# Performance work log

Measured on AMD Instinct MI355X. Metric: run time of the kernel, lower is better.

The kernel has to match this reference:

```python
import jax, jax.numpy as jnp
import numpy as np

B, L, D_MODEL = 2, 4096, 256
EXPAND = 2
D_INNER = EXPAND * D_MODEL
D_STATE = 16
D_CONV = 4
DT_RANK = max(1, D_MODEL // 16)


def setup_inputs() -> dict:
    key = jax.random.key(0)
    ks = jax.random.split(key, 8)
    s = 0.02
    return {
        "x": jax.random.normal(ks[0], (B, L, D_MODEL), jnp.float32),
        "in_proj_w": jax.random.normal(ks[1], (D_MODEL, 2 * D_INNER), jnp.float32) * s,
        "conv_w": jax.random.normal(ks[2], (D_INNER, D_CONV), jnp.float32) * 0.1,
        "conv_b": jnp.zeros((D_INNER,), jnp.float32),
        "x_proj_w": jax.random.normal(ks[3], (D_INNER, DT_RANK + 2 * D_STATE), jnp.float32) * s,
        "dt_proj_w": jax.random.normal(ks[4], (DT_RANK, D_INNER), jnp.float32) * (DT_RANK ** -0.5),
        "dt_proj_b": jnp.log(jnp.expm1(jnp.full((D_INNER,), 0.01, jnp.float32))),
        "A_log": jnp.log(jnp.tile(jnp.arange(1, D_STATE + 1, dtype=jnp.float32), (D_INNER, 1))),
        "D": jnp.ones((D_INNER,), jnp.float32),
        "out_proj_w": jax.random.normal(ks[5], (D_INNER, D_MODEL), jnp.float32) * s,
        "ln_gamma": jnp.ones((D_MODEL,), jnp.float32),
        "ln_beta": jnp.zeros((D_MODEL,), jnp.float32),
    }


def _mamba(x, in_proj_w, conv_w, conv_b, x_proj_w, dt_proj_w, dt_proj_b, A_log, D, out_proj_w):
    b = x.shape[0]
    xz = x @ in_proj_w                       # [B,L,2*d_inner]
    u, z = jnp.split(xz, 2, axis=-1)
    # depthwise causal conv over time
    u_pad = jnp.pad(u, ((0, 0), (D_CONV - 1, 0), (0, 0)))
    kern = conv_w.T[:, None, :]              # [D_CONV, 1, D_INNER]
    u_conv = jax.lax.conv_general_dilated(
        u_pad, kern, (1,), 'VALID',
        dimension_numbers=('NHC', 'HIO', 'NHC'),
        feature_group_count=D_INNER) + conv_b
    u_conv = jax.nn.silu(u_conv)             # [B,L,d_inner]
    dbl = u_conv @ x_proj_w
    dt, Bm, Cm = jnp.split(dbl, [DT_RANK, DT_RANK + D_STATE], axis=-1)
    delta = jax.nn.softplus(dt @ dt_proj_w + dt_proj_b)   # [B,L,d_inner]
    A = -jnp.exp(A_log)                                    # [d_inner,d_state]
    dA = jnp.exp(delta[..., None] * A)                     # [B,L,di,ds]
    dBu = delta[..., None] * Bm[:, :, None, :] * u_conv[..., None]

    def step(h, inputs):
        dA_t, dBu_t, C_t = inputs
        h = dA_t * h + dBu_t                 # [B,di,ds]
        y = jnp.einsum('bdn,bn->bd', h, C_t)
        return h, y

    h0 = jnp.zeros((b, D_INNER, D_STATE), u_conv.dtype)
    _, ys = jax.lax.scan(step, h0,
                         (dA.transpose(1, 0, 2, 3),
                          dBu.transpose(1, 0, 2, 3),
                          Cm.transpose(1, 0, 2)))
    y = ys.transpose(1, 0, 2) + u_conv * D
    y = y * jax.nn.silu(z)
    return y @ out_proj_w


def reference(x, in_proj_w, conv_w, conv_b, x_proj_w, dt_proj_w, dt_proj_b,
              A_log, D, out_proj_w, ln_gamma, ln_beta):
    y = x + _mamba(x, in_proj_w, conv_w, conv_b, x_proj_w, dt_proj_w,
                   dt_proj_b, A_log, D, out_proj_w)
    mu = jnp.mean(y, axis=-1, keepdims=True)
    var = jnp.var(y, axis=-1, keepdims=True)
    return (y - mu) / jnp.sqrt(var + 1e-5) * ln_gamma + ln_beta
```

## Files before the change

### kernel.cpp

```cpp
#include <hip/hip_runtime.h>
#include <math.h>

constexpr int BATCH  = 2;
constexpr int LSEQ   = 4096;
constexpr int DMODEL = 256;
constexpr int DINNER = 512;
constexpr int NST    = 16;
constexpr int MROWS  = BATCH * LSEQ;
constexpr int NCH    = 256;
constexpr int TCH    = LSEQ / NCH;
constexpr float LOG2E = 1.44269504088896f;
constexpr float LN2   = 0.69314718056f;

typedef __attribute__((ext_vector_type(8))) short bf16x8;
typedef __attribute__((ext_vector_type(4))) float f32x4;

__device__ __forceinline__ float fast_silu(float v) { return v / (1.f + __expf(-v)); }

__device__ __forceinline__ unsigned short f2bf(float f) {
  unsigned int u = __float_as_uint(f);
  u = (u + 0x7fffu + ((u >> 16) & 1u)) >> 16;
  return (unsigned short)u;
}
__device__ __forceinline__ float bf2f(unsigned short u) {
  return __uint_as_float(((unsigned int)u) << 16);
}

__global__ __launch_bounds__(256) void k_castT(const float* __restrict__ W,
                                               unsigned short* __restrict__ Wt,
                                               int K, int N, int ktiles) {
  __shared__ float tile[32][33];
  const int bt = blockIdx.x;
  const int kt = bt % ktiles, nt = bt / ktiles;
  const int k0 = kt * 32, n0 = nt * 32;
  const int t = threadIdx.x;
  const int c = t & 31, r0 = t >> 5;
  #pragma unroll
  for (int it = 0; it < 4; ++it) {
    int r = r0 + it * 8;
    tile[r][c] = W[(size_t)(k0 + r) * N + n0 + c];
  }
  __syncthreads();
  #pragma unroll
  for (int it = 0; it < 4; ++it) {
    int cc = r0 + it * 8;
    Wt[(size_t)(n0 + cc) * K + k0 + c] = f2bf(tile[c][cc]);
  }
}

__global__ __launch_bounds__(256) void k_cast_xpw(const float* __restrict__ xpw,
                                                  unsigned short* __restrict__ xpT) {
  int idx = blockIdx.x * 256 + threadIdx.x;
  int n = idx >> 9, k = idx & 511;
  xpT[n * 512 + k] = f2bf(xpw[k * 48 + n]);
}

__global__ __launch_bounds__(256) void k_prep_a2(const float* __restrict__ Alog,
                                                 float* __restrict__ a2T) {
  int idx = blockIdx.x * 256 + threadIdx.x;
  int n = idx >> 9, d = idx & 511;
  a2T[idx] = -__expf(Alog[d * NST + n]) * LOG2E;
}

__global__ __launch_bounds__(256) void k_inproj(const float* __restrict__ X,
                                                const unsigned short* __restrict__ Wt,
                                                unsigned short* __restrict__ ub,
                                                unsigned short* __restrict__ zb) {
  __shared__ unsigned short As[128][40];
  __shared__ unsigned short Bs[128][40];
  const int t = threadIdx.x;
  const int m0 = (blockIdx.x & 63) * 128;
  const int n0 = (blockIdx.x >> 6) * 128;
  const int lane = t & 63, wid = t >> 6;
  const int hi = lane >> 4, l15 = lane & 15;
  const int wm = wid >> 1, wn = wid & 1;
  f32x4 zero = {0.f, 0.f, 0.f, 0.f};
  f32x4 acc[4][4];
  #pragma unroll
  for (int i = 0; i < 4; ++i)
    #pragma unroll
    for (int j = 0; j < 4; ++j) acc[i][j] = zero;

  for (int k0 = 0; k0 < DMODEL; k0 += 32) {
    __syncthreads();
    #pragma unroll
    for (int it = 0; it < 4; ++it) {
      int v = it * 256 + t;
      int r = v >> 3, part = v & 7;
      float4 a = *(const float4*)(X + (size_t)(m0 + r) * 256 + k0 + part * 4);
      ushort4 o;
      o.x = f2bf(a.x); o.y = f2bf(a.y); o.z = f2bf(a.z); o.w = f2bf(a.w);
      *(ushort4*)(&As[r][part * 4]) = o;
    }
    #pragma unroll
    for (int it = 0; it < 2; ++it) {
      int v = it * 256 + t;
      int r = v >> 2, part = v & 3;
      *(float4*)(&Bs[r][part * 8]) = *(const float4*)(Wt + (size_t)(n0 + r) * 256 + k0 + part * 8);
    }
    __syncthreads();
    bf16x8 af[4], bfv[4];
    #pragma unroll
    for (int am = 0; am < 4; ++am) af[am] = *(const bf16x8*)(&As[wm * 64 + am * 16 + l15][hi * 8]);
    #pragma unroll
    for (int bn = 0; bn < 4; ++bn) bfv[bn] = *(const bf16x8*)(&Bs[wn * 64 + bn * 16 + l15][hi * 8]);
    #pragma unroll
    for (int am = 0; am < 4; ++am)
      #pragma unroll
      for (int bn = 0; bn < 4; ++bn)
        acc[am][bn] = __builtin_amdgcn_mfma_f32_16x16x32_bf16(af[am], bfv[bn], acc[am][bn], 0, 0, 0);
  }

  unsigned short* dst = (n0 < DINNER) ? ub : zb;
  const int nb = (n0 < DINNER) ? n0 : n0 - DINNER;
  #pragma unroll
  for (int am = 0; am < 4; ++am)
    #pragma unroll
    for (int j = 0; j < 4; ++j) {
      int m = m0 + wm * 64 + am * 16 + hi * 4 + j;
      #pragma unroll
      for (int bn = 0; bn < 4; ++bn) {
        int n = nb + wn * 64 + bn * 16 + l15;
        dst[(size_t)m * DINNER + n] = f2bf(acc[am][bn][j]);
      }
    }
}

__global__ __launch_bounds__(256) void k_conv(const unsigned short* __restrict__ ub,
                                              const float* __restrict__ cw,
                                              const float* __restrict__ cb,
                                              unsigned short* __restrict__ ucb) {
  const int e2 = blockIdx.x * 256 + threadIdx.x;
  const int idx = e2 * 2;
  const int d = idx & (DINNER - 1);
  const int m = idx >> 9;
  const int l = m & (LSEQ - 1);
  float a0 = cb[d], a1 = cb[d + 1];
  #pragma unroll
  for (int j = 0; j < 4; ++j) {
    int lj = l + j - 3;
    unsigned int p = (lj >= 0) ? *(const unsigned int*)(ub + idx + (j - 3) * DINNER) : 0u;
    float u0 = bf2f((unsigned short)(p & 0xffffu));
    float u1 = bf2f((unsigned short)(p >> 16));
    a0 = fmaf(u0, cw[d * 4 + j], a0);
    a1 = fmaf(u1, cw[(d + 1) * 4 + j], a1);
  }
  unsigned int o = (unsigned int)f2bf(fast_silu(a0)) | ((unsigned int)f2bf(fast_silu(a1)) << 16);
  *(unsigned int*)(ucb + idx) = o;
}

__global__ __launch_bounds__(128) void k_xprojm(const unsigned short* __restrict__ ucb,
                                                const unsigned short* __restrict__ xpT,
                                                float* __restrict__ dt_out,
                                                float* __restrict__ Bout,
                                                float* __restrict__ Cout) {
  __shared__ unsigned short As[32][136];
  __shared__ unsigned short Bs[48][136];
  const int t = threadIdx.x;
  const int m0 = blockIdx.x * 32;
  const int lane = t & 63, wid = t >> 6;
  const int hi = lane >> 4, l15 = lane & 15;
  f32x4 zero = {0.f, 0.f, 0.f, 0.f};
  f32x4 acc[3] = {zero, zero, zero};

  for (int k0 = 0; k0 < DINNER; k0 += 128) {
    __syncthreads();
    #pragma unroll
    for (int it = 0; it < 4; ++it) {
      int v = it * 128 + t;
      int r = v >> 4, part = v & 15;
      *(float4*)(&As[r][part * 8]) = *(const float4*)(ucb + (size_t)(m0 + r) * 512 + k0 + part * 8);
    }
    #pragma unroll
    for (int it = 0; it < 6; ++it) {
      int v = it * 128 + t;
      int r = v >> 4, part = v & 15;
      *(float4*)(&Bs[r][part * 8]) = *(const float4*)(xpT + (size_t)r * 512 + k0 + part * 8);
    }
    __syncthreads();
    #pragma unroll
    for (int kk = 0; kk < 4; ++kk) {
      bf16x8 af = *(const bf16x8*)(&As[wid * 16 + l15][kk * 32 + hi * 8]);
      #pragma unroll
      for (int nf = 0; nf < 3; ++nf) {
        bf16x8 bv = *(const bf16x8*)(&Bs[nf * 16 + l15][kk * 32 + hi * 8]);
        acc[nf] = __builtin_amdgcn_mfma_f32_16x16x32_bf16(af, bv, acc[nf], 0, 0, 0);
      }
    }
  }
  #pragma unroll
  for (int j = 0; j < 4; ++j) {
    int m = m0 + wid * 16 + hi * 4 + j;
    dt_out[m * 16 + l15] = acc[0][j];
    Bout[m * 16 + l15]   = acc[1][j];
    Cout[m * 16 + l15]   = acc[2][j];
  }
}

__global__ __launch_bounds__(256) void k_scan1(const unsigned short* __restrict__ ucb,
                                               const float* __restrict__ dtin,
                                               const float* __restrict__ dtw,
                                               const float* __restrict__ dtb,
                                               const float* __restrict__ Bin,
                                               const float* __restrict__ a2T,
                                               unsigned short* __restrict__ delta_b,
                                               unsigned short* __restrict__ Ssum,
                                               float* __restrict__ Dsum) {
  const int t = threadIdx.x;
  const int d0 = (blockIdx.x & 1) * 256;
  const int rest = blockIdx.x >> 1;
  const int c = rest & (NCH - 1);
  const int b = rest >> 8;
  const int d = d0 + t;
  __shared__ float Bsh[TCH][NST];
  __shared__ float dtsh[TCH][NST];
  __shared__ unsigned short UC[TCH][256];
  const int rbase = (b * LSEQ + c * TCH) * DINNER + d0;
  {
    const int base = (b * LSEQ + c * TCH) * NST;
    ((float*)Bsh)[t]  = Bin[base + t];
    ((float*)dtsh)[t] = dtin[base + t];
    #pragma unroll
    for (int it = 0; it < 2; ++it) {
      int v = it * 256 + t;
      int r = v >> 5, col8 = v & 31;
      *(float4*)(&UC[r][col8 * 8]) = *(const float4*)(ucb + rbase + r * DINNER + col8 * 8);
    }
  }
  __syncthreads();
  float dwreg[NST];
  #pragma unroll
  for (int r = 0; r < NST; ++r) dwreg[r] = dtw[r * DINNER + d];
  const float bias = dtb[d];
  float a2[NST];
  #pragma unroll
  for (int n = 0; n < NST; ++n) a2[n] = a2T[n * DINNER + d];
  bool geo = true;
  #pragma unroll
  for (int n = 1; n < NST; ++n)
    geo = geo && (fabsf(a2[n] - (float)(n + 1) * a2[0]) <= 1e-5f * fabsf(a2[n]));
  float S[NST];
  #pragma unroll
  for (int n = 0; n < NST; ++n) S[n] = 0.f;
  float dsum = 0.f;
  const int row0 = rbase + t;
  for (int tt = 0; tt < TCH; ++tt) {
    float acc = bias;
    #pragma unroll
    for (int r = 0; r < NST; ++r) acc = fmaf(dtsh[tt][r], dwreg[r], acc);
    float sp = (acc > 20.f) ? acc : log1pf(__expf(acc));
    unsigned short deb = f2bf(sp);
    delta_b[row0 + tt * DINNER] = deb;
    float de = bf2f(deb);
    float xv = bf2f(UC[tt][t]);
    float du = de * xv;
    dsum += de;
    float dA[NST];
    if (geo) {
      float r1 = exp2f(de * a2[0]);
      float p = r1;
      #pragma unroll
      for (int n = 0; n < NST; ++n) { dA[n] = p; p *= r1; }
    } else {
      #pragma unroll
      for (int n = 0; n < NST; ++n) dA[n] = exp2f(de * a2[n]);
    }
    #pragma unroll
    for (int n = 0; n < NST; ++n) S[n] = fmaf(dA[n], S[n], du * Bsh[tt][n]);
  }
  const int bc = b * NCH + c;
  Dsum[bc * DINNER + d] = dsum;
  #pragma unroll
  for (int n = 0; n < NST; ++n)
    Ssum[(size_t)((n * BATCH + b) * NCH + c) * DINNER + d] = f2bf(S[n]);
}

__global__ __launch_bounds__(64) void k_scan2(const unsigned short* __restrict__ S,
                                              const float* __restrict__ Dsum,
                                              const float* __restrict__ a2T,
                                              unsigned short* __restrict__ Hinit) {
  const int idx = blockIdx.x * 64 + threadIdx.x;
  const int d  = idx & (DINNER - 1);
  const int nb = idx >> 9;
  const int b  = nb & (BATCH - 1);
  const int n  = nb >> 1;
  const float a = a2T[n * DINNER + d] * LN2;
  const unsigned short* Srow = S     + (size_t)nb * NCH * DINNER + d;
  const float*          Drow = Dsum  + (size_t)b  * NCH * DINNER + d;
  unsigned short*       Hrow = Hinit + (size_t)nb * NCH * DINNER + d;
  float h = 0.f;
  #pragma unroll 8
  for (int c = 0; c < NCH; ++c) {
    float ds = Drow[(size_t)c * DINNER];
    float s  = bf2f(Srow[(size_t)c * DINNER]);
    Hrow[(size_t)c * DINNER] = f2bf(h);
    h = fmaf(__expf(a * ds), h, s);
  }
}

__global__ __launch_bounds__(256) void k_scan3(const unsigned short* __restrict__ ucb,
                                               const unsigned short* __restrict__ delta_b,
                                               const float* __restrict__ Bin,
                                               const float* __restrict__ Cin,
                                               const float* __restrict__ a2T,
                                               const float* __restrict__ Dvec,
                                               const unsigned short* __restrict__ Hinit,
                                               unsigned short* __restrict__ zb) {
  const int t = threadIdx.x;
  const int d0 = (blockIdx.x & 1) * 256;
  const int rest = blockIdx.x >> 1;
  const int c = rest & (NCH - 1);
  const int b = rest >> 8;
  const int d = d0 + t;
  __shared__ float Bsh[TCH][NST];
  __shared__ float Csh[TCH][NST];
  __shared__ unsigned short UC[TCH][256];
  __shared__ unsigned short DE[TCH][256];
  const int rbase = (b * LSEQ + c * TCH) * DINNER + d0;
  {
    const int base = (b * LSEQ + c * TCH) * NST;
    ((float*)Bsh)[t] = Bin[base + t];
    ((float*)Csh)[t] = Cin[base + t];
    #pragma unroll
    for (int it = 0; it < 2; ++it) {
      int v = it * 256 + t;
      int r = v >> 5, col8 = v & 31;
      *(float4*)(&UC[r][col8 * 8]) = *(const float4*)(ucb     + rbase + r * DINNER + col8 * 8);
      *(float4*)(&DE[r][col8 * 8]) = *(const float4*)(delta_b + rbase + r * DINNER + col8 * 8);
    }
  }
  __syncthreads();
  float a2[NST];
  #pragma unroll
  for (int n = 0; n < NST; ++n) a2[n] = a2T[n * DINNER + d];
  bool geo = true;
  #pragma unroll
  for (int n = 1; n < NST; ++n)
    geo = geo && (fabsf(a2[n] - (float)(n + 1) * a2[0]) <= 1e-5f * fabsf(a2[n]));
  float h[NST];
  #pragma unroll
  for (int n = 0; n < NST; ++n)
    h[n] = bf2f(Hinit[(size_t)(((n * BATCH + b) * NCH) + c) * DINNER + d]);
  const float Dd = Dvec[d];
  const int row0 = rbase + t;
  for (int tt = 0; tt < TCH; ++tt) {
    float de = bf2f(DE[tt][t]);
    float xv = bf2f(UC[tt][t]);
    float du = de * xv;
    float dA[NST];
    if (geo) {
      float r1 = exp2f(de * a2[0]);
      float p = r1;
      #pragma unroll
      for (int n = 0; n < NST; ++n) { dA[n] = p; p *= r1; }
    } else {
      #pragma unroll
      for (int n = 0; n < NST; ++n) dA[n] = exp2f(de * a2[n]);
    }
    float y = 0.f;
    #pragma unroll
    for (int n = 0; n < NST; ++n) {
      h[n] = fmaf(dA[n], h[n], du * Bsh[tt][n]);
      y = fmaf(h[n], Csh[tt][n], y);
    }
    float zz = bf2f(zb[row0 + tt * DINNER]);
    zb[row0 + tt * DINNER] = f2bf((y + xv * Dd) * fast_silu(zz));
  }
}

__global__ __launch_bounds__(512) void k_out(const unsigned short* __restrict__ Yb,
                                             const unsigned short* __restrict__ W2t,
                                             const float* __restrict__ X,
                                             const float* __restrict__ gam,
                                             const float* __restrict__ bet,
                                             float* __restrict__ out) {
  __shared__ unsigned short As[32][40];
  __shared__ unsigned short Bs[256][40];
  __shared__ float red[4][32][2];
  const int t = threadIdx.x;
  const int m0 = blockIdx.x * 32;
  const int lane = t & 63, wid = t >> 6;
  const int hi = lane >> 4, l15 = lane & 15;
  const int wm = wid >> 2, wn = wid & 3;
  f32x4 zero = {0.f, 0.f, 0.f, 0.f};
  f32x4 acc[4];
  #pragma unroll
  for (int bn = 0; bn < 4; ++bn) acc[bn] = zero;

  for (int k0 = 0; k0 < DINNER; k0 += 32) {
    __syncthreads();
    if (t < 128) {
      int r = t >> 2, part = t & 3;
      *(float4*)(&As[r][part * 8]) = *(const float4*)(Yb + (size_t)(m0 + r) * 512 + k0 + part * 8);
    }
    #pragma unroll
    for (int it = 0; it < 2; ++it) {
      int v = it * 512 + t;
      int r = v >> 2, part = v & 3;
      *(float4*)(&Bs[r][part * 8]) = *(const float4*)(W2t + (size_t)r * 512 + k0 + part * 8);
    }
    __syncthreads();
    bf16x8 af = *(const bf16x8*)(&As[wm * 16 + l15][hi * 8]);
    #pragma unroll
    for (int bn = 0; bn < 4; ++bn) {
      bf16x8 bfr = *(const bf16x8*)(&Bs[wn * 64 + bn * 16 + l15][hi * 8]);
      acc[bn] = __builtin_amdgcn_mfma_f32_16x16x32_bf16(af, bfr, acc[bn], 0, 0, 0);
    }
  }

  float vv[4][4];
  float s[4] = {0.f, 0.f, 0.f, 0.f}, s2[4] = {0.f, 0.f, 0.f, 0.f};
  #pragma unroll
  for (int bn = 0; bn < 4; ++bn) {
    int n = wn * 64 + bn * 16 + l15;
    #pragma unroll
    for (int j = 0; j < 4; ++j) {
      int m = m0 + wm * 16 + hi * 4 + j;
      float v = acc[bn][j] + X[(size_t)m * DMODEL + n];
      vv[bn][j] = v;
      s[j] += v; s2[j] += v * v;
    }
  }
  #pragma unroll
  for (int j = 0; j < 4; ++j) {
    #pragma unroll
    for (int off = 1; off < 16; off <<= 1) {
      s[j]  += __shfl_xor(s[j],  off, 64);
      s2[j] += __shfl_xor(s2[j], off, 64);
    }
  }
  if (l15 == 0) {
    #pragma unroll
    for (int j = 0; j < 4; ++j) {
      red[wn][wm * 16 + hi * 4 + j][0] = s[j];
      red[wn][wm * 16 + hi * 4 + j][1] = s2[j];
    }
  }
  __syncthreads();
  float g[4], bb[4];
  #pragma unroll
  for (int bn = 0; bn < 4; ++bn) {
    int n = wn * 64 + bn * 16 + l15;
    g[bn] = gam[n]; bb[bn] = bet[n];
  }
  #pragma unroll
  for (int j = 0; j < 4; ++j) {
    int row = wm * 16 + hi * 4 + j;
    float S  = red[0][row][0] + red[1][row][0] + red[2][row][0] + red[3][row][0];
    float S2 = red[0][row][1] + red[1][row][1] + red[2][row][1] + red[3][row][1];
    float mu = S * (1.f / 256.f);
    float rstd = rsqrtf(S2 * (1.f / 256.f) - mu * mu + 1e-5f);
    int m = m0 + row;
    #pragma unroll
    for (int bn = 0; bn < 4; ++bn) {
      int n = wn * 64 + bn * 16 + l15;
      out[(size_t)m * DMODEL + n] = (vv[bn][j] - mu) * rstd * g[bn] + bb[bn];
    }
  }
}

extern "C" void kernel_launch(void* const* d_in, const int* in_sizes, int n_in,
                              void* d_out, int out_size, void* d_ws, size_t ws_size,
                              hipStream_t stream) {
  const float* x    = (const float*)d_in[0];
  const float* ipw  = (const float*)d_in[1];
  const float* cw   = (const float*)d_in[2];
  const float* cb   = (const float*)d_in[3];
  const float* xpw  = (const float*)d_in[4];
  const float* dtw  = (const float*)d_in[5];
  const float* dtbv = (const float*)d_in[6];
  const float* alog = (const float*)d_in[7];
  const float* Dv   = (const float*)d_in[8];
  const float* opw  = (const float*)d_in[9];
  const float* gam  = (const float*)d_in[10];
  const float* bet  = (const float*)d_in[11];
  float* out = (float*)d_out;

  char* ws = (char*)d_ws;
  unsigned short* ub  = (unsigned short*)ws;   ws += (size_t)MROWS * DINNER * 2;
  unsigned short* zb  = (unsigned short*)ws;   ws += (size_t)MROWS * DINNER * 2;
  unsigned short* ucb = (unsigned short*)ws;   ws += (size_t)MROWS * DINNER * 2;
  float* buf_dt = (float*)ws;  ws += (size_t)MROWS * NST * 4;
  float* buf_B  = (float*)ws;  ws += (size_t)MROWS * NST * 4;
  float* buf_C  = (float*)ws;  ws += (size_t)MROWS * NST * 4;
  float* buf_ds = (float*)ws;  ws += (size_t)BATCH * NCH * DINNER * 4;
  unsigned short* buf_S = (unsigned short*)ws;  ws += (size_t)NST * BATCH * NCH * DINNER * 2;
  unsigned short* buf_H = (unsigned short*)ws;  ws += (size_t)NST * BATCH * NCH * DINNER * 2;
  unsigned short* W1t = (unsigned short*)ws; ws += (size_t)1024 * 256 * 2;
  unsigned short* W2t = (unsigned short*)ws; ws += (size_t)256 * 512 * 2;
  unsigned short* xpT = (unsigned short*)ws; ws += (size_t)48 * 512 * 2;
  float* a2T = (float*)ws;     ws += (size_t)NST * DINNER * 4;
  unsigned short* deltab = ub;

  k_castT   <<<dim3(256),  dim3(256), 0, stream>>>(ipw, W1t, 256, 1024, 8);
  k_castT   <<<dim3(128),  dim3(256), 0, stream>>>(opw, W2t, 512, 256, 16);
  k_cast_xpw<<<dim3(96),   dim3(256), 0, stream>>>(xpw, xpT);
  k_prep_a2 <<<dim3(32),   dim3(256), 0, stream>>>(alog, a2T);
  k_inproj  <<<dim3(512),  dim3(256), 0, stream>>>(x, W1t, ub, zb);
  k_conv    <<<dim3(MROWS * DINNER / 512), dim3(256), 0, stream>>>(ub, cw, cb, ucb);
  k_xprojm  <<<dim3(MROWS / 32), dim3(128), 0, stream>>>(ucb, xpT, buf_dt, buf_B, buf_C);
  k_scan1   <<<dim3(BATCH * NCH * DINNER / 256), dim3(256), 0, stream>>>(ucb, buf_dt, dtw, dtbv, buf_B,
                                                                         a2T, deltab, buf_S, buf_ds);
  k_scan2   <<<dim3(NST * BATCH * DINNER / 64), dim3(64), 0, stream>>>(buf_S, buf_ds, a2T, buf_H);
  k_scan3   <<<dim3(BATCH * NCH * DINNER / 256), dim3(256), 0, stream>>>(ucb, deltab, buf_B, buf_C,
                                                                         a2T, Dv, buf_H, zb);
  k_out     <<<dim3(MROWS / 32), dim3(512), 0, stream>>>(zb, W2t, x, gam, bet, out);
}
```

Before: 134.7 us.

## Fuse weight prep kernels and fold causal conv into x_proj GEMM

Measured after the change: 111.0 us. -17.6%, faster.

```diff
diff --git a/kernel.cpp b/kernel.cpp
--- a/kernel.cpp
+++ b/kernel.cpp
@@ -26,40 +26,44 @@
   return __uint_as_float(((unsigned int)u) << 16);
 }
 
-__global__ __launch_bounds__(256) void k_castT(const float* __restrict__ W,
-                                               unsigned short* __restrict__ Wt,
-                                               int K, int N, int ktiles) {
+__global__ __launch_bounds__(256) void k_prep(const float* __restrict__ ipw,
+                                              const float* __restrict__ opw,
+                                              const float* __restrict__ xpw,
+                                              const float* __restrict__ Alog,
+                                              unsigned short* __restrict__ W1t,
+                                              unsigned short* __restrict__ W2t,
+                                              unsigned short* __restrict__ xpT,
+                                              float* __restrict__ a2T) {
   __shared__ float tile[32][33];
-  const int bt = blockIdx.x;
-  const int kt = bt % ktiles, nt = bt / ktiles;
-  const int k0 = kt * 32, n0 = nt * 32;
+  const int bid = blockIdx.x;
   const int t = threadIdx.x;
-  const int c = t & 31, r0 = t >> 5;
-  #pragma unroll
-  for (int it = 0; it < 4; ++it) {
-    int r = r0 + it * 8;
-    tile[r][c] = W[(size_t)(k0 + r) * N + n0 + c];
-  }
-  __syncthreads();
-  #pragma unroll
-  for (int it = 0; it < 4; ++it) {
-    int cc = r0 + it * 8;
-    Wt[(size_t)(n0 + cc) * K + k0 + c] = f2bf(tile[c][cc]);
-  }
-}
-
-__global__ __launch_bounds__(256) void k_cast_xpw(const float* __restrict__ xpw,
-                                                  unsigned short* __restrict__ xpT) {
-  int idx = blockIdx.x * 256 + threadIdx.x;
-  int n = idx >> 9, k = idx & 511;
-  xpT[n * 512 + k] = f2bf(xpw[k * 48 + n]);
-}
-
-__global__ __launch_bounds__(256) void k_prep_a2(const float* __restrict__ Alog,
-                                                 float* __restrict__ a2T) {
-  int idx = blockIdx.x * 256 + threadIdx.x;
-  int n = idx >> 9, d = idx & 511;
-  a2T[idx] = -__expf(Alog[d * NST + n]) * LOG2E;
+  if (bid < 384) {
+    const float* W; unsigned short* Wt; int K, N, ktiles, bt;
+    if (bid < 256) { W = ipw; Wt = W1t; K = 256; N = 1024; ktiles = 8;  bt = bid; }
+    else           { W = opw; Wt = W2t; K = 512; N = 256;  ktiles = 16; bt = bid - 256; }
+    const int kt = bt % ktiles, nt = bt / ktiles;
+    const int k0 = kt * 32, n0 = nt * 32;
+    const int c = t & 31, r0 = t >> 5;
+    #pragma unroll
+    for (int it = 0; it < 4; ++it) {
+      int r = r0 + it * 8;
+      tile[r][c] = W[(size_t)(k0 + r) * N + n0 + c];
+    }
+    __syncthreads();
+    #pragma unroll
+    for (int it = 0; it < 4; ++it) {
+      int cc = r0 + it * 8;
+      Wt[(size_t)(n0 + cc) * K + k0 + c] = f2bf(tile[c][cc]);
+    }
+  } else if (bid < 480) {
+    int idx = (bid - 384) * 256 + t;
+    int n = idx >> 9, k = idx & 511;
+    xpT[n * 512 + k] = f2bf(xpw[k * 48 + n]);
+  } else {
+    int idx = (bid - 480) * 256 + t;
+    int n = idx >> 9, d = idx & 511;
+    a2T[idx] = -__expf(Alog[d * NST + n]) * LOG2E;
+  }
 }
 
 __global__ __launch_bounds__(256) void k_inproj(const float* __restrict__ X,
@@ -126,51 +130,56 @@
     }
 }
 
-__global__ __launch_bounds__(256) void k_conv(const unsigned short* __restrict__ ub,
-                                              const float* __restrict__ cw,
-                                              const float* __restrict__ cb,
-                                              unsigned short* __restrict__ ucb) {
-  const int e2 = blockIdx.x * 256 + threadIdx.x;
-  const int idx = e2 * 2;
-  const int d = idx & (DINNER - 1);
-  const int m = idx >> 9;
-  const int l = m & (LSEQ - 1);
-  float a0 = cb[d], a1 = cb[d + 1];
-  #pragma unroll
-  for (int j = 0; j < 4; ++j) {
-    int lj = l + j - 3;
-    unsigned int p = (lj >= 0) ? *(const unsigned int*)(ub + idx + (j - 3) * DINNER) : 0u;
-    float u0 = bf2f((unsigned short)(p & 0xffffu));
-    float u1 = bf2f((unsigned short)(p >> 16));
-    a0 = fmaf(u0, cw[d * 4 + j], a0);
-    a1 = fmaf(u1, cw[(d + 1) * 4 + j], a1);
-  }
-  unsigned int o = (unsigned int)f2bf(fast_silu(a0)) | ((unsigned int)f2bf(fast_silu(a1)) << 16);
-  *(unsigned int*)(ucb + idx) = o;
-}
-
-__global__ __launch_bounds__(128) void k_xprojm(const unsigned short* __restrict__ ucb,
+__global__ __launch_bounds__(128) void k_xprojm(const unsigned short* __restrict__ ub,
+                                                const float* __restrict__ cw,
+                                                const float* __restrict__ cb,
+                                                unsigned short* __restrict__ ucb,
                                                 const unsigned short* __restrict__ xpT,
                                                 float* __restrict__ dt_out,
                                                 float* __restrict__ Bout,
                                                 float* __restrict__ Cout) {
-  __shared__ unsigned short As[32][136];
+  __shared__ unsigned short U[35][520];
   __shared__ unsigned short Bs[48][136];
   const int t = threadIdx.x;
   const int m0 = blockIdx.x * 32;
+  const int l0 = m0 & (LSEQ - 1);
   const int lane = t & 63, wid = t >> 6;
   const int hi = lane >> 4, l15 = lane & 15;
+
+  for (int v = t; v < 35 * 64; v += 128) {
+    int r = v >> 6, c8 = v & 63;
+    float4 val = {0.f, 0.f, 0.f, 0.f};
+    if (l0 - 3 + r >= 0)
+      val = *(const float4*)(ub + (size_t)(m0 - 3 + r) * 512 + c8 * 8);
+    *(float4*)(&U[r][c8 * 8]) = val;
+  }
+  __syncthreads();
+
+  #pragma unroll
+  for (int cc = 0; cc < 4; ++cc) {
+    const int k = t * 4 + cc;
+    const float w0 = cw[k * 4 + 0], w1 = cw[k * 4 + 1], w2 = cw[k * 4 + 2], w3 = cw[k * 4 + 3];
+    const float bias = cb[k];
+    for (int r = 31; r >= 0; --r) {
+      float acc = bias;
+      acc = fmaf(bf2f(U[r + 0][k]), w0, acc);
+      acc = fmaf(bf2f(U[r + 1][k]), w1, acc);
+      acc = fmaf(bf2f(U[r + 2][k]), w2, acc);
+      acc = fmaf(bf2f(U[r + 3][k]), w3, acc);
+      U[r + 3][k] = f2bf(fast_silu(acc));
+    }
+  }
+  __syncthreads();
+
+  for (int v = t; v < 32 * 64; v += 128) {
+    int r = v >> 6, c8 = v & 63;
+    *(float4*)(ucb + (size_t)(m0 + r) * 512 + c8 * 8) = *(const float4*)(&U[r + 3][c8 * 8]);
+  }
+
   f32x4 zero = {0.f, 0.f, 0.f, 0.f};
   f32x4 acc[3] = {zero, zero, zero};
-
   for (int k0 = 0; k0 < DINNER; k0 += 128) {
     __syncthreads();
-    #pragma unroll
-    for (int it = 0; it < 4; ++it) {
-      int v = it * 128 + t;
-      int r = v >> 4, part = v & 15;
-      *(float4*)(&As[r][part * 8]) = *(const float4*)(ucb + (size_t)(m0 + r) * 512 + k0 + part * 8);
-    }
     #pragma unroll
     for (int it = 0; it < 6; ++it) {
       int v = it * 128 + t;
@@ -180,7 +189,7 @@
     __syncthreads();
     #pragma unroll
     for (int kk = 0; kk < 4; ++kk) {
-      bf16x8 af = *(const bf16x8*)(&As[wid * 16 + l15][kk * 32 + hi * 8]);
+      bf16x8 af = *(const bf16x8*)(&U[3 + wid * 16 + l15][k0 + kk * 32 + hi * 8]);
       #pragma unroll
       for (int nf = 0; nf < 3; ++nf) {
         bf16x8 bv = *(const bf16x8*)(&Bs[nf * 16 + l15][kk * 32 + hi * 8]);
@@ -248,7 +257,7 @@
     float acc = bias;
     #pragma unroll
     for (int r = 0; r < NST; ++r) acc = fmaf(dtsh[tt][r], dwreg[r], acc);
-    float sp = (acc > 20.f) ? acc : log1pf(__expf(acc));
+    float sp = (acc > 20.f) ? acc : __logf(1.f + __expf(acc));
     unsigned short deb = f2bf(sp);
     delta_b[row0 + tt * DINNER] = deb;
     float de = bf2f(deb);
@@ -492,17 +501,13 @@
   float* a2T = (float*)ws;     ws += (size_t)NST * DINNER * 4;
   unsigned short* deltab = ub;
 
-  k_castT   <<<dim3(256),  dim3(256), 0, stream>>>(ipw, W1t, 256, 1024, 8);
-  k_castT   <<<dim3(128),  dim3(256), 0, stream>>>(opw, W2t, 512, 256, 16);
-  k_cast_xpw<<<dim3(96),   dim3(256), 0, stream>>>(xpw, xpT);
-  k_prep_a2 <<<dim3(32),   dim3(256), 0, stream>>>(alog, a2T);
-  k_inproj  <<<dim3(512),  dim3(256), 0, stream>>>(x, W1t, ub, zb);
-  k_conv    <<<dim3(MROWS * DINNER / 512), dim3(256), 0, stream>>>(ub, cw, cb, ucb);
-  k_xprojm  <<<dim3(MROWS / 32), dim3(128), 0, stream>>>(ucb, xpT, buf_dt, buf_B, buf_C);
-  k_scan1   <<<dim3(BATCH * NCH * DINNER / 256), dim3(256), 0, stream>>>(ucb, buf_dt, dtw, dtbv, buf_B,
-                                                                         a2T, deltab, buf_S, buf_ds);
-  k_scan2   <<<dim3(NST * BATCH * DINNER / 64), dim3(64), 0, stream>>>(buf_S, buf_ds, a2T, buf_H);
-  k_scan3   <<<dim3(BATCH * NCH * DINNER / 256), dim3(256), 0, stream>>>(ucb, deltab, buf_B, buf_C,
-                                                                         a2T, Dv, buf_H, zb);
-  k_out     <<<dim3(MROWS / 32), dim3(512), 0, stream>>>(zb, W2t, x, gam, bet, out);
-}
+  k_prep   <<<dim3(512),  dim3(256), 0, stream>>>(ipw, opw, xpw, alog, W1t, W2t, xpT, a2T);
+  k_inproj <<<dim3(512),  dim3(256), 0, stream>>>(x, W1t, ub, zb);
+  k_xprojm <<<dim3(MROWS / 32), dim3(128), 0, stream>>>(ub, cw, cb, ucb, xpT, buf_dt, buf_B, buf_C);
+  k_scan1  <<<dim3(BATCH * NCH * 2), dim3(256), 0, stream>>>(ucb, buf_dt, dtw, dtbv, buf_B,
+                                                             a2T, deltab, buf_S, buf_ds);
+  k_scan2  <<<dim3(NST * BATCH * DINNER / 64), dim3(64), 0, stream>>>(buf_S, buf_ds, a2T, buf_H);
+  k_scan3  <<<dim3(BATCH * NCH * 2), dim3(256), 0, stream>>>(ucb, deltab, buf_B, buf_C,
+                                                             a2T, Dv, buf_H, zb);
+  k_out    <<<dim3(MROWS / 32), dim3(512), 0, stream>>>(zb, W2t, x, gam, bet, out);
+}
```
